# Optimization experiments

Measured on AMD Instinct MI355X. Metric: run time of the kernel, lower is better.

## Reference

```python
import jax, jax.numpy as jnp
import numpy as np

B, T, I, H = 2048, 256, 64, 64  # batch, seq_len, input_size, hidden_size


def setup_inputs() -> dict:
    key = jax.random.key(0)
    ks = jax.random.split(key, 11)
    w = lambda k, shape: (jax.random.normal(k, shape, jnp.float32) * 0.05)
    return {
        "x": jax.random.normal(ks[0], (B, T, I), jnp.float32),
        # layer 0 (input -> hidden), PyTorch gate order [i, f, g, o] stacked along dim 0
        "W_ih0": w(ks[1], (4 * H, I)),
        "W_hh0": w(ks[2], (4 * H, H)),
        "b_ih0": w(ks[3], (4 * H,)),
        "b_hh0": w(ks[4], (4 * H,)),
        # layer 1 (hidden -> hidden)
        "W_ih1": w(ks[5], (4 * H, H)),
        "W_hh1": w(ks[6], (4 * H, H)),
        "b_ih1": w(ks[7], (4 * H,)),
        "b_hh1": w(ks[8], (4 * H,)),
        # final projection hidden -> 1
        "fc_w": w(ks[9], (1, H)),
        "fc_b": w(ks[10], (1,)),
    }


def _lstm_layer(x, W_ih, W_hh, b_ih, b_hh):
    """Single LSTM layer, batch_first input (B, T, D) -> (B, T, H).
    PyTorch gate order: i, f, g, o."""
    Bsz, Tlen, _ = x.shape
    Hd = W_hh.shape[1]
    # Precompute input projections for all timesteps in one big GEMM.
    x_proj = jnp.einsum("btd,gd->btg", x, W_ih) + b_ih + b_hh  # (B, T, 4H)
    x_proj = jnp.swapaxes(x_proj, 0, 1)  # (T, B, 4H) for scan over time

    def step(carry, xt):
        h, c = carry
        gates = xt + h @ W_hh.T  # (B, 4H)
        i, f, g, o = jnp.split(gates, 4, axis=-1)
        i = jax.nn.sigmoid(i)
        f = jax.nn.sigmoid(f)
        g = jnp.tanh(g)
        o = jax.nn.sigmoid(o)
        c = f * c + i * g
        h = o * jnp.tanh(c)
        return (h, c), h

    h0 = jnp.zeros((Bsz, Hd), x.dtype)
    (_, _), hs = jax.lax.scan(step, (h0, h0), x_proj)
    return jnp.swapaxes(hs, 0, 1)  # (B, T, H)


def reference(x, W_ih0, W_hh0, b_ih0, b_hh0, W_ih1, W_hh1, b_ih1, b_hh1, fc_w, fc_b):
    # Dropout between layers is inactive in eval mode -> omitted.
    h1 = _lstm_layer(x, W_ih0, W_hh0, b_ih0, b_hh0)
    h2 = _lstm_layer(h1, W_ih1, W_hh1, b_ih1, b_hh1)
    last_hidden = h2[:, -1, :]  # (B, H)
    out = last_hidden @ fc_w.T + fc_b  # (B, 1)
    return out[:, 0]  # squeeze(-1) -> (B,)
```

## Files before the change

kernel.cpp:

```cpp
#include <hip/hip_runtime.h>

typedef short short8 __attribute__((ext_vector_type(8)));
typedef float f32x4  __attribute__((ext_vector_type(4)));
typedef unsigned short u16;

#define T_LEN 256
#define NB    8
#define GRID  (2048 / NB)
#define LDK   72

static __device__ __forceinline__ u16 bf16_rne(float f) {
    unsigned u = __builtin_bit_cast(unsigned, f);
    return (u16)((u + 0x7fffu + ((u >> 16) & 1u)) >> 16);
}
static __device__ __forceinline__ float bf16_f(u16 h) {
    unsigned u = ((unsigned)h) << 16;
    return __builtin_bit_cast(float, u);
}
static __device__ __forceinline__ void split_tr(float f, u16& hi, u16& lo) {
    unsigned u = __builtin_bit_cast(unsigned, f);
    hi = (u16)(u >> 16);
    float rest = f - __builtin_bit_cast(float, u & 0xffff0000u);
    lo = (u16)(__builtin_bit_cast(unsigned, rest) >> 16);
}
static __device__ __forceinline__ float fast_sigmoid(float x) {
    float e = __builtin_amdgcn_exp2f(x * -1.4426950408889634f);
    return __builtin_amdgcn_rcpf(1.0f + e);
}
static __device__ __forceinline__ float fast_tanh(float x) {
    float e = __builtin_amdgcn_exp2f(x * -2.8853900817779268f);
    return 2.0f * __builtin_amdgcn_rcpf(1.0f + e) - 1.0f;
}

__global__ __launch_bounds__(1024)
void lstm2_mfma(const float* __restrict__ x,
                const float* __restrict__ W_ih0, const float* __restrict__ W_hh0,
                const float* __restrict__ b_ih0, const float* __restrict__ b_hh0,
                const float* __restrict__ W_ih1, const float* __restrict__ W_hh1,
                const float* __restrict__ b_ih1, const float* __restrict__ b_hh1,
                const float* __restrict__ fc_w,  const float* __restrict__ fc_b,
                float* __restrict__ out)
{
    const int tid = threadIdx.x;
    const int l   = tid & 63;
    const int w   = tid >> 6;
    const int grp = w >> 3;
    const int wl  = w & 7;
    const int ln  = l & 15;
    const int kg  = l >> 4;

    __shared__ __align__(16) u16 XB[2][16][LDK];
    __shared__ __align__(16) u16 H1[2][16][LDK];
    __shared__ __align__(16) u16 H2[2][16][LDK];
    __shared__ __align__(16) float hfin[NB][68];

    short8 Ah[2][4], Al[2][4];
    f32x4  biasv[2];
    {
        const float* Wi = grp ? W_ih1 : W_ih0;
        const float* Wh = grp ? W_hh1 : W_hh0;
        const float* bi = grp ? b_ih1 : b_ih0;
        const float* bh = grp ? b_hh1 : b_hh0;
        #pragma unroll
        for (int mt = 0; mt < 2; ++mt) {
            #pragma unroll
            for (int kt = 0; kt < 4; ++kt) {
                const int uu   = ln >> 2;
                const int gate = ln & 3;
                const int row  = gate * 64 + (wl * 8 + mt * 4 + uu);
                const int kb   = kt * 32 + kg * 8;
                const float* src = (kb < 64) ? (Wi + (size_t)row * 64 + kb)
                                             : (Wh + (size_t)row * 64 + (kb - 64));
                short8 h8, l8;
                #pragma unroll
                for (int j = 0; j < 8; ++j) {
                    float v = src[j];
                    u16 hh = bf16_rne(v);
                    u16 ll = bf16_rne(v - bf16_f(hh));
                    h8[j] = (short)hh; l8[j] = (short)ll;
                }
                Ah[mt][kt] = h8; Al[mt][kt] = l8;
            }
            f32x4 bv;
            #pragma unroll
            for (int r = 0; r < 4; ++r) {
                const int row = r * 64 + (wl * 8 + mt * 4 + kg);
                bv[r] = bi[row] + bh[row];
            }
            biasv[mt] = bv;
        }
    }

    {
        u16* p0 = &XB[0][0][0];
        u16* p1 = &H1[0][0][0];
        u16* p2 = &H2[0][0][0];
        const int tot = 2 * 16 * LDK;
        for (int i = tid; i < tot; i += 1024) { p0[i] = 0; p1[i] = 0; p2[i] = 0; }
    }
    __syncthreads();

    const int    sb    = blockIdx.x * NB;
    const int    xs    = (tid >> 6) & 7;
    const int    xj    = tid & 63;
    const bool   stg   = (tid < 512);
    const size_t xbase = ((size_t)(sb + xs)) * T_LEN * 64 + xj;

    if (stg) {
        u16 hh, ll; split_tr(x[xbase], hh, ll);
        XB[0][xs][xj]     = hh;
        XB[0][8 + xs][xj] = ll;
    }
    __syncthreads();

    const int  mtl  = (ln >> 3) & 1;
    const int  smp  = ln & 7;
    const int  un   = wl * 8 + mtl * 4 + kg;
    const bool lo8  = (ln < 8);
    float cstate = 0.f;
    float xcur = stg ? x[xbase + 64] : 0.f;

#define MFMA(A, B, C) __builtin_amdgcn_mfma_f32_16x16x32_bf16(A, B, C, 0, 0, 0)

    #pragma unroll 1
    for (int t = 0; t <= T_LEN; ++t) {
        const int p = t & 1, q = p ^ 1;
        float xnext = 0.f;
        if (stg && t + 2 < T_LEN) xnext = x[xbase + (size_t)(t + 2) * 64];

        const bool active = grp ? (t >= 1) : (t < T_LEN);
        if (active) {
            const u16 (*BA)[LDK] = grp ? H1[p] : XB[p];
            const u16 (*BB)[LDK] = grp ? H2[p] : H1[p];
            short8 b0 = *(const short8*)&BA[ln][kg * 8];
            short8 b1 = *(const short8*)&BA[ln][32 + kg * 8];
            short8 b2 = *(const short8*)&BB[ln][kg * 8];
            short8 b3 = *(const short8*)&BB[ln][32 + kg * 8];

            __builtin_amdgcn_s_setprio(1);
            f32x4 aH0 = {0.f, 0.f, 0.f, 0.f}, aH1 = {0.f, 0.f, 0.f, 0.f};
            f32x4 aL0 = biasv[0],             aL1 = biasv[1];
            aH0 = MFMA(Ah[0][0], b0, aH0);  aH1 = MFMA(Ah[1][0], b0, aH1);
            aL0 = MFMA(Al[0][0], b0, aL0);  aL1 = MFMA(Al[1][0], b0, aL1);
            aH0 = MFMA(Ah[0][1], b1, aH0);  aH1 = MFMA(Ah[1][1], b1, aH1);
            aL0 = MFMA(Al[0][1], b1, aL0);  aL1 = MFMA(Al[1][1], b1, aL1);
            aH0 = MFMA(Ah[0][2], b2, aH0);  aH1 = MFMA(Ah[1][2], b2, aH1);
            aL0 = MFMA(Al[0][2], b2, aL0);  aL1 = MFMA(Al[1][2], b2, aL1);
            aH0 = MFMA(Ah[0][3], b3, aH0);  aH1 = MFMA(Ah[1][3], b3, aH1);
            aL0 = MFMA(Al[0][3], b3, aL0);  aL1 = MFMA(Al[1][3], b3, aL1);
            __builtin_amdgcn_s_setprio(0);

            f32x4 pk;
            #pragma unroll
            for (int r = 0; r < 4; ++r) {
                float send = lo8 ? (aH1[r] + aL1[r]) : aH0[r];
                float recv = __shfl_xor(send, 8, 64);
                pk[r] = lo8 ? (aH0[r] + recv + aL0[r])
                            : (aH1[r] + recv);
            }
            const float ig = fast_sigmoid(pk[0]);
            const float fg = fast_sigmoid(pk[1]);
            const float gg = fast_tanh(pk[2]);
            const float og = fast_sigmoid(pk[3]);
            const float cc = fg * cstate + ig * gg;
            cstate = cc;
            const float hv = og * fast_tanh(cc);

            u16 hh, ll; split_tr(hv, hh, ll);
            if (grp == 0) {
                H1[q][smp][un]     = hh;
                H1[q][8 + smp][un] = ll;
            } else {
                H2[q][smp][un]     = hh;
                H2[q][8 + smp][un] = ll;
                if (t == T_LEN) hfin[smp][un] = hv;
            }
        }

        if (stg && t + 1 < T_LEN) {
            u16 hh, ll; split_tr(xcur, hh, ll);
            XB[q][xs][xj]     = hh;
            XB[q][8 + xs][xj] = ll;
        }
        xcur = xnext;
        __syncthreads();
    }
#undef MFMA

    if (w < 8) {
        float v = hfin[w][l] * fc_w[l];
        #pragma unroll
        for (int off = 32; off; off >>= 1) v += __shfl_xor(v, off, 64);
        if (l == 0) out[sb + w] = v + fc_b[0];
    }
}

extern "C" void kernel_launch(void* const* d_in, const int* in_sizes, int n_in,
                              void* d_out, int out_size, void* d_ws, size_t ws_size,
                              hipStream_t stream) {
    const float* x     = (const float*)d_in[0];
    const float* W_ih0 = (const float*)d_in[1];
    const float* W_hh0 = (const float*)d_in[2];
    const float* b_ih0 = (const float*)d_in[3];
    const float* b_hh0 = (const float*)d_in[4];
    const float* W_ih1 = (const float*)d_in[5];
    const float* W_hh1 = (const float*)d_in[6];
    const float* b_ih1 = (const float*)d_in[7];
    const float* b_hh1 = (const float*)d_in[8];
    const float* fc_w  = (const float*)d_in[9];
    const float* fc_b  = (const float*)d_in[10];
    float* out = (float*)d_out;

    lstm2_mfma<<<GRID, 1024, 0, stream>>>(x, W_ih0, W_hh0, b_ih0, b_hh0,
                                          W_ih1, W_hh1, b_ih1, b_hh1,
                                          fc_w, fc_b, out);
}
```

Baseline: 283.0 us.

## Move x staging to layer-1 waves, unroll time loop by two with precomputed LDS pointers

Reassigns the per-step x load and bf16 split/store from the layer-0 waves to the layer-1 waves, so the layer-0 critical path no longer carries staging work. The time loop is unrolled by two with precomputed double-buffer LDS pointers, which removes the per-step parity index arithmetic. The x staging store is placed between the B-operand loads and the MFMA chain so it can overlap. The setprio hints are dropped, which may change wave scheduling.

```diff
diff --git a/kernel.cpp b/kernel.cpp
--- a/kernel.cpp
+++ b/kernel.cpp
@@ -101,9 +101,9 @@
     __syncthreads();
 
     const int    sb    = blockIdx.x * NB;
-    const int    xs    = (tid >> 6) & 7;
-    const int    xj    = tid & 63;
-    const bool   stg   = (tid < 512);
+    const bool   stg   = (grp == 1);
+    const int    xs    = wl;
+    const int    xj    = l;
     const size_t xbase = ((size_t)(sb + xs)) * T_LEN * 64 + xj;
 
     if (stg) {
@@ -119,72 +119,76 @@
     const bool lo8  = (ln < 8);
     float cstate = 0.f;
     float xcur = stg ? x[xbase + 64] : 0.f;
+    const float* xp = x + xbase + 2 * 64;
+
+    const u16* rdA0 = grp ? &H1[0][ln][kg * 8] : &XB[0][ln][kg * 8];
+    const u16* rdA1 = grp ? &H1[1][ln][kg * 8] : &XB[1][ln][kg * 8];
+    const u16* rdB0 = grp ? &H2[0][ln][kg * 8] : &H1[0][ln][kg * 8];
+    const u16* rdB1 = grp ? &H2[1][ln][kg * 8] : &H1[1][ln][kg * 8];
+    u16* wr0 = grp ? &H2[0][smp][un] : &H1[0][smp][un];
+    u16* wr1 = grp ? &H2[1][smp][un] : &H1[1][smp][un];
+    u16* sx0 = &XB[0][xs][xj];
+    u16* sx1 = &XB[1][xs][xj];
 
 #define MFMA(A, B, C) __builtin_amdgcn_mfma_f32_16x16x32_bf16(A, B, C, 0, 0, 0)
 
+#define STEP(T, rdA, rdB, wrh, sxh)                                          \
+    do {                                                                     \
+        const bool act_ = grp ? ((T) >= 1) : ((T) < T_LEN);                  \
+        float xnext_ = 0.f;                                                  \
+        if (stg && (T) + 2 < T_LEN) xnext_ = *xp;                            \
+        short8 b0, b1, b2, b3;                                               \
+        if (act_) {                                                          \
+            b0 = *(const short8*)(rdA);                                      \
+            b1 = *(const short8*)((rdA) + 32);                               \
+            b2 = *(const short8*)(rdB);                                      \
+            b3 = *(const short8*)((rdB) + 32);                               \
+        }                                                                    \
+        if (stg && (T) + 1 < T_LEN) {              \
+            u16 hh_, ll_; split_tr(xcur, hh_, ll_);                          \
+            (sxh)[0] = hh_; (sxh)[8 * LDK] = ll_;                            \
+        }                                                                    \
+        if (act_) {                                                          \
+            f32x4 aH0 = {0.f,0.f,0.f,0.f}, aH1 = {0.f,0.f,0.f,0.f};          \
+            f32x4 aL0 = biasv[0],          aL1 = biasv[1];                   \
+            aH0 = MFMA(Ah[0][0], b0, aH0);  aH1 = MFMA(Ah[1][0], b0, aH1);   \
+            aL0 = MFMA(Al[0][0], b0, aL0);  aL1 = MFMA(Al[1][0], b0, aL1);   \
+            aH0 = MFMA(Ah[0][1], b1, aH0);  aH1 = MFMA(Ah[1][1], b1, aH1);   \
+            aL0 = MFMA(Al[0][1], b1, aL0);  aL1 = MFMA(Al[1][1], b1, aL1);   \
+            aH0 = MFMA(Ah[0][2], b2, aH0);  aH1 = MFMA(Ah[1][2], b2, aH1);   \
+            aL0 = MFMA(Al[0][2], b2, aL0);  aL1 = MFMA(Al[1][2], b2, aL1);   \
+            aH0 = MFMA(Ah[0][3], b3, aH0);  aH1 = MFMA(Ah[1][3], b3, aH1);   \
+            aL0 = MFMA(Al[0][3], b3, aL0);  aL1 = MFMA(Al[1][3], b3, aL1);   \
+            f32x4 pk;                                                        \
+            _Pragma("unroll")                                                \
+            for (int r = 0; r < 4; ++r) {                                    \
+                float send = lo8 ? (aH1[r] + aL1[r]) : aH0[r];               \
+                float recv = __shfl_xor(send, 8, 64);                        \
+                pk[r] = lo8 ? (aH0[r] + recv + aL0[r]) : (aH1[r] + recv);    \
+            }                                                                \
+            const float ig = fast_sigmoid(pk[0]);                            \
+            const float fg = fast_sigmoid(pk[1]);                            \
+            const float gg = fast_tanh(pk[2]);                               \
+            const float og = fast_sigmoid(pk[3]);                            \
+            const float cc = fg * cstate + ig * gg;                          \
+            cstate = cc;                                                     \
+            const float hv = og * fast_tanh(cc);                             \
+            u16 hh_, ll_; split_tr(hv, hh_, ll_);                            \
+            (wrh)[0] = hh_; (wrh)[8 * LDK] = ll_;                            \
+            if (grp && (T) == T_LEN) hfin[smp][un] = hv;                     \
+        }                                                                    \
+        xcur = xnext_;                                                       \
+        xp += 64;                                                            \
+        __syncthreads();                                                     \
+    } while (0)
+
+    STEP(0, rdA0, rdB0, wr1, sx1);
     #pragma unroll 1
-    for (int t = 0; t <= T_LEN; ++t) {
-        const int p = t & 1, q = p ^ 1;
-        float xnext = 0.f;
-        if (stg && t + 2 < T_LEN) xnext = x[xbase + (size_t)(t + 2) * 64];
-
-        const bool active = grp ? (t >= 1) : (t < T_LEN);
-        if (active) {
-            const u16 (*BA)[LDK] = grp ? H1[p] : XB[p];
-            const u16 (*BB)[LDK] = grp ? H2[p] : H1[p];
-            short8 b0 = *(const short8*)&BA[ln][kg * 8];
-            short8 b1 = *(const short8*)&BA[ln][32 + kg * 8];
-            short8 b2 = *(const short8*)&BB[ln][kg * 8];
-            short8 b3 = *(const short8*)&BB[ln][32 + kg * 8];
-
-            __builtin_amdgcn_s_setprio(1);
-            f32x4 aH0 = {0.f, 0.f, 0.f, 0.f}, aH1 = {0.f, 0.f, 0.f, 0.f};
-            f32x4 aL0 = biasv[0],             aL1 = biasv[1];
-            aH0 = MFMA(Ah[0][0], b0, aH0);  aH1 = MFMA(Ah[1][0], b0, aH1);
-            aL0 = MFMA(Al[0][0], b0, aL0);  aL1 = MFMA(Al[1][0], b0, aL1);
-            aH0 = MFMA(Ah[0][1], b1, aH0);  aH1 = MFMA(Ah[1][1], b1, aH1);
-            aL0 = MFMA(Al[0][1], b1, aL0);  aL1 = MFMA(Al[1][1], b1, aL1);
-            aH0 = MFMA(Ah[0][2], b2, aH0);  aH1 = MFMA(Ah[1][2], b2, aH1);
-            aL0 = MFMA(Al[0][2], b2, aL0);  aL1 = MFMA(Al[1][2], b2, aL1);
-            aH0 = MFMA(Ah[0][3], b3, aH0);  aH1 = MFMA(Ah[1][3], b3, aH1);
-            aL0 = MFMA(Al[0][3], b3, aL0);  aL1 = MFMA(Al[1][3], b3, aL1);
-            __builtin_amdgcn_s_setprio(0);
-
-            f32x4 pk;
-            #pragma unroll
-            for (int r = 0; r < 4; ++r) {
-                float send = lo8 ? (aH1[r] + aL1[r]) : aH0[r];
-                float recv = __shfl_xor(send, 8, 64);
-                pk[r] = lo8 ? (aH0[r] + recv + aL0[r])
-                            : (aH1[r] + recv);
-            }
-            const float ig = fast_sigmoid(pk[0]);
-            const float fg = fast_sigmoid(pk[1]);
-            const float gg = fast_tanh(pk[2]);
-            const float og = fast_sigmoid(pk[3]);
-            const float cc = fg * cstate + ig * gg;
-            cstate = cc;
-            const float hv = og * fast_tanh(cc);
-
-            u16 hh, ll; split_tr(hv, hh, ll);
-            if (grp == 0) {
-                H1[q][smp][un]     = hh;
-                H1[q][8 + smp][un] = ll;
-            } else {
-                H2[q][smp][un]     = hh;
-                H2[q][8 + smp][un] = ll;
-                if (t == T_LEN) hfin[smp][un] = hv;
-            }
-        }
-
-        if (stg && t + 1 < T_LEN) {
-            u16 hh, ll; split_tr(xcur, hh, ll);
-            XB[q][xs][xj]     = hh;
-            XB[q][8 + xs][xj] = ll;
-        }
-        xcur = xnext;
-        __syncthreads();
-    }
+    for (int t = 1; t < T_LEN; t += 2) {
+        STEP(t,     rdA1, rdB1, wr0, sx0);
+        STEP(t + 1, rdA0, rdB0, wr1, sx1);
+    }
+#undef STEP
 #undef MFMA
 
     if (w < 8) {
```

Result: slower. 493.0 us (+74.2%).
